# Optimization experiments

Hardware: AMD Instinct MI355X
Metric: run time of the kernel (lower is better)

Reference implementation:

```python
import jax, jax.numpy as jnp
import numpy as np

HEAD_DIM = 128  # dim // num_heads; RoPE rot_dim and softmax scale
ROPE_THETA = 10000.0


def rope_rotate(x, rot_dim):
    # lucidrains RotaryEmbedding.rotate_queries_or_keys: rotate first rot_dim
    # channels of last axis with interleaved-pair rotation; pass rest through.
    T = x.shape[-2]
    inv_freq = 1.0 / (ROPE_THETA ** (jnp.arange(0, rot_dim, 2, dtype=jnp.float32) / rot_dim))
    freqs = jnp.arange(T, dtype=jnp.float32)[:, None] * inv_freq[None, :]  # [T, rot_dim//2]
    freqs = jnp.repeat(freqs, 2, axis=-1)  # [T, rot_dim] interleaved (f0,f0,f1,f1,...)
    cos, sin = jnp.cos(freqs), jnp.sin(freqs)
    xr, x_pass = x[..., :rot_dim], x[..., rot_dim:]
    x1, x2 = xr[..., 0::2], xr[..., 1::2]
    rot = jnp.stack([-x2, x1], axis=-1).reshape(xr.shape)  # rotate_half
    xr = xr * cos + rot * sin
    return jnp.concatenate([xr, x_pass], axis=-1)


def setup_inputs() -> dict:
    key = jax.random.key(0)
    ks = jax.random.split(key, 9)
    B, T, D = 2, 2048, 2048
    w = lambda k, shape: jax.random.normal(k, shape, dtype=jnp.float32) * 0.02
    return {
        "latent_space": jax.random.normal(ks[0], (B, T, D), dtype=jnp.float32),
        "Wq": w(ks[1], (D, D)), "bq": w(ks[2], (D,)),
        "Wk": w(ks[3], (D, D)), "bk": w(ks[4], (D,)),
        "Wv": w(ks[5], (D, D)), "bv": w(ks[6], (D,)),
        "Wfc": w(ks[7], (D, D)), "bfc": w(ks[8], (D,)),
    }


def reference(latent_space, Wq, bq, Wk, bk, Wv, bv, Wfc, bfc):
    # Projections (nn.Linear: x @ W.T + b)
    Q = latent_space @ Wq.T + bq
    K = latent_space @ Wk.T + bk
    V = latent_space @ Wv.T + bv
    # Fused RoPE on first HEAD_DIM channels (module never splits heads)
    Q = rope_rotate(Q, HEAD_DIM)
    K = rope_rotate(K, HEAD_DIM)
    # Full-hidden-dim QK^T: [B,T,T]
    qk = jnp.einsum('btd,bsd->bts', Q, K)
    T = qk.shape[-1]
    causal = jnp.triu(jnp.ones((T, T), dtype=bool), 1)
    A = jnp.where(causal, -jnp.inf, qk)
    # PartialSoftmax with temp=1, h_t=None: state = A/sqrt(head_dim);
    # out = exp(state)/sum(exp(state)) * 2
    state = A / jnp.sqrt(jnp.float32(HEAD_DIM))
    x_exp = jnp.exp(state)
    A = x_exp / jnp.sum(x_exp, axis=-1, keepdims=True) * 2.0
    out = jnp.einsum('bts,bsd->btd', A, V) @ Wfc.T + bfc
    return out
```

## Files before the change

kernel.cpp:

```cpp
#include <hip/hip_runtime.h>
#include <hip/hip_bf16.h>
#include <math.h>

using bf16 = __hip_bfloat16;
typedef __attribute__((ext_vector_type(8))) __bf16 bf16x8;
typedef __attribute__((ext_vector_type(4))) float f32x4;

#define SBAR() asm volatile("s_barrier" ::: "memory")
#define WAITVM(n) asm volatile("s_waitcnt vmcnt(" #n ")" ::: "memory")

static __device__ __forceinline__ void gload16(const bf16* g, bf16* l) {
  __builtin_amdgcn_global_load_lds((const __attribute__((address_space(1))) void*)g,
                                   (__attribute__((address_space(3))) void*)l, 16, 0, 0);
}

struct POff { long a[4]; long b[4]; long c[4]; const float* bias[4]; };
struct CvtP { const float* s[5]; bf16* d[5]; int n4[5]; };

__global__ __launch_bounds__(256) void cvt_f32_bf16(CvtP p) {
  const int y = blockIdx.y;
  const int i = blockIdx.x * 256 + threadIdx.x;
  if (i >= p.n4[y]) return;
  const float4 v = reinterpret_cast<const float4*>(p.s[y])[i];
  union { bf16 h[4]; short4 s4; } u;
  u.h[0] = __float2bfloat16(v.x);
  u.h[1] = __float2bfloat16(v.y);
  u.h[2] = __float2bfloat16(v.z);
  u.h[3] = __float2bfloat16(v.w);
  *reinterpret_cast<short4*>(p.d[y] + 4 * (size_t)i) = u.s4;
}

template<bool BIAS, bool F32OUT, bool CAUSAL, bool KTRUNC>
__global__ __launch_bounds__(512, 2) void gemm_nt(
    const bf16* __restrict__ A, const bf16* __restrict__ B, char* __restrict__ Cv,
    POff P, int K, int lda, int ldb, int ldc)
{
  if (CAUSAL && (int)blockIdx.x > 2 * (int)blockIdx.y + 1) return;
  const int z = blockIdx.z;
  A = (const bf16*)((const char*)A + P.a[z]);
  B = (const bf16*)((const char*)B + P.b[z]);
  char* C = Cv + P.c[z];
  const int by = KTRUNC ? ((int)gridDim.y - 1 - (int)blockIdx.y) : (int)blockIdx.y;
  const int rowBase = by * 256;
  const int colBase = blockIdx.x * 128;
  const int tid  = threadIdx.x;
  const int lane = tid & 63;
  const int wid  = tid >> 6;
  const int wm = wid >> 1;
  const int wn = wid & 1;
  const int kEnd = KTRUNC ? (rowBase + 256) : K;
  const int NT = kEnd >> 5;

  __shared__ alignas(16) bf16 ls[4][12288];

  f32x4 acc[4][4] = {};

  const int rt  = tid >> 2;
  const int sw8 = ((tid & 3) ^ ((rt >> 1) & 3)) * 8;
  const bf16* gA0 = A + (size_t)(rowBase + rt) * lda + sw8;
  const bf16* gA1 = gA0 + (size_t)128 * lda;
  const bf16* gB0 = B + (size_t)(colBase + rt) * ldb + sw8;

  const int lr = lane >> 4, lc = lane & 15;
  const int kb = (lr ^ ((lc >> 1) & 3)) * 8;

#define STAGE(t) { bf16* d = &ls[(t) & 3][0]; const int ko = (t) * 32; \
    gload16(gA0 + ko, &d[tid * 8]); \
    gload16(gA1 + ko, &d[4096 + tid * 8]); \
    gload16(gB0 + ko, &d[8192 + tid * 8]); }

  STAGE(0); STAGE(1); STAGE(2);

  for (int t = 0; t < NT; ++t) {
    if (t < NT - 2)       WAITVM(6);
    else if (t == NT - 2) WAITVM(3);
    else                  WAITVM(0);
    SBAR();
    const bf16* LA = &ls[t & 3][0];
    const bf16* LB = &ls[t & 3][8192];
    bf16x8 af[4], bfr[4];
#pragma unroll
    for (int m = 0; m < 4; ++m)
      af[m] = *reinterpret_cast<const bf16x8*>(&LA[(wm * 64 + m * 16 + lc) * 32 + kb]);
#pragma unroll
    for (int n = 0; n < 4; ++n)
      bfr[n] = *reinterpret_cast<const bf16x8*>(&LB[(wn * 64 + n * 16 + lc) * 32 + kb]);
    if (t + 3 < NT) STAGE(t + 3);
    SBAR();
    __builtin_amdgcn_s_setprio(1);
#pragma unroll
    for (int m = 0; m < 4; ++m)
#pragma unroll
      for (int n = 0; n < 4; ++n)
        acc[m][n] = __builtin_amdgcn_mfma_f32_16x16x32_bf16(af[m], bfr[n], acc[m][n], 0, 0, 0);
    __builtin_amdgcn_s_setprio(0);
  }
#undef STAGE

  const float* bias = P.bias[z];
  const int crow0 = rowBase + wm * 64;
  const int ccol0 = colBase + wn * 64;
#pragma unroll
  for (int m = 0; m < 4; ++m) {
    const int row0 = crow0 + m * 16 + lr * 4;
#pragma unroll
    for (int n = 0; n < 4; ++n) {
      const int col = ccol0 + n * 16 + lc;
      const float bv = BIAS ? bias[col] : 0.f;
#pragma unroll
      for (int j = 0; j < 4; ++j) {
        const float v = acc[m][n][j] + bv;
        const long idx = (long)(row0 + j) * ldc + col;
        if (F32OUT) reinterpret_cast<float*>(C)[idx] = v;
        else        reinterpret_cast<bf16*>(C)[idx] = __float2bfloat16(v);
      }
    }
  }
}

__global__ __launch_bounds__(256) void rope_bf16(bf16* __restrict__ X) {
  const int idx = blockIdx.x * 256 + threadIdx.x;
  const int row = idx >> 6;
  const int i   = idx & 63;
  const int t   = row & 2047;
  const float ang = (float)t * exp2f((float)i * -0.20762050593046f);
  float sn, cs;
  sincosf(ang, &sn, &cs);
  bf16* p = X + ((long)row << 11) + 2 * i;
  const float x1 = __bfloat162float(p[0]);
  const float x2 = __bfloat162float(p[1]);
  p[0] = __float2bfloat16(x1 * cs - x2 * sn);
  p[1] = __float2bfloat16(x2 * cs + x1 * sn);
}

__global__ __launch_bounds__(256) void softmax_causal(
    const float* __restrict__ S0, const float* __restrict__ S1,
    const float* __restrict__ S2, const float* __restrict__ S3,
    bf16* __restrict__ A0, bf16* __restrict__ A1) {
  const int t = blockIdx.x;
  const int b = blockIdx.y;
  const float* ra = (b ? S2 : S0) + (long)t * 2048;
  const float* rb = (b ? S3 : S1) + (long)t * 2048;
  bf16* orow = (b ? A1 : A0) + (long)t * 4096;
  const int L = t + 1;
  __shared__ float e[2048];
  __shared__ float red[4];
  const float scale = 0.0883883476483184f;
  const int lane = threadIdx.x & 63, wd = threadIdx.x >> 6;

  float mx = -INFINITY;
  for (int s = threadIdx.x; s < L; s += 256) {
    const float v = (ra[s] + rb[s]) * scale;
    e[s] = v;
    mx = fmaxf(mx, v);
  }
#pragma unroll
  for (int off = 1; off < 64; off <<= 1) mx = fmaxf(mx, __shfl_xor(mx, off));
  if (lane == 0) red[wd] = mx;
  __syncthreads();
  mx = fmaxf(fmaxf(red[0], red[1]), fmaxf(red[2], red[3]));
  __syncthreads();

  float sum = 0.f;
  for (int s = threadIdx.x; s < L; s += 256) {
    const float v = expf(e[s] - mx);
    e[s] = v;
    sum += v;
  }
#pragma unroll
  for (int off = 1; off < 64; off <<= 1) sum += __shfl_xor(sum, off);
  if (lane == 0) red[wd] = sum;
  __syncthreads();
  sum = red[0] + red[1] + red[2] + red[3];
  const float f = 2.f / sum;
  for (int s = threadIdx.x; s < 2048; s += 256) {
    const float v = (s < L) ? e[s] * f : 0.f;
    orow[s] = __float2bfloat16(v);
  }
}

__global__ __launch_bounds__(256) void transpose_bf16(
    const bf16* __restrict__ V, bf16* __restrict__ VT) {
  __shared__ bf16 tile[32][33];
  const long b = blockIdx.z;
  const int s0 = blockIdx.y * 32, d0 = blockIdx.x * 32;
  const int tx = threadIdx.x;
  const int ty = threadIdx.y;
  for (int i = ty; i < 32; i += 8)
    tile[i][tx] = V[(b * 2048 + s0 + i) * 2048 + d0 + tx];
  __syncthreads();
  for (int i = ty; i < 32; i += 8)
    VT[(b * 2048 + d0 + i) * 2048 + s0 + tx] = tile[tx][i];
}

extern "C" void kernel_launch(void* const* d_in, const int* in_sizes, int n_in,
                              void* d_out, int out_size, void* d_ws, size_t ws_size,
                              hipStream_t stream) {
  (void)in_sizes; (void)n_in; (void)out_size; (void)ws_size;
  const float* lat = (const float*)d_in[0];
  const float* Wq  = (const float*)d_in[1];
  const float* bq  = (const float*)d_in[2];
  const float* Wk  = (const float*)d_in[3];
  const float* bk  = (const float*)d_in[4];
  const float* Wv  = (const float*)d_in[5];
  const float* bv  = (const float*)d_in[6];
  const float* Wfc = (const float*)d_in[7];
  const float* bfc = (const float*)d_in[8];
  float* out = (float*)d_out;

  constexpr long T = 2048, D = 2048, MT = 4096;
  constexpr long TTB = T * T * 4;
  char* w = (char*)d_ws;
  bf16* latb = (bf16*)w;  w += MT * D * 2;
  bf16* wqb  = (bf16*)w;  w += D * D * 2;
  bf16* wkb  = (bf16*)w;  w += D * D * 2;
  bf16* wvb  = (bf16*)w;  w += D * D * 2;
  bf16* wfb  = (bf16*)w;  w += D * D * 2;
  bf16* Qb   = (bf16*)w;  w += MT * D * 2;
  bf16* Kb   = (bf16*)w;  w += MT * D * 2;
  bf16* Vb   = (bf16*)w;  w += MT * D * 2;
  bf16* VTb  = (bf16*)w;  w += MT * D * 2;
  float* S0  = (float*)w; w += TTB;
  float* S1  = (float*)w; w += TTB;
  float* S2  = (float*)d_out;
  float* S3  = (float*)((char*)d_out + TTB);
  bf16* A0   = (bf16*)S0;
  bf16* A1   = (bf16*)S3;
  bf16* Ob   = latb;

  CvtP cp;
  cp.s[0] = lat; cp.d[0] = latb; cp.n4[0] = (int)(MT * D / 4);
  cp.s[1] = Wq;  cp.d[1] = wqb;  cp.n4[1] = (int)(D * D / 4);
  cp.s[2] = Wk;  cp.d[2] = wkb;  cp.n4[2] = (int)(D * D / 4);
  cp.s[3] = Wv;  cp.d[3] = wvb;  cp.n4[3] = (int)(D * D / 4);
  cp.s[4] = Wfc; cp.d[4] = wfb;  cp.n4[4] = (int)(D * D / 4);
  cvt_f32_bf16<<<dim3(8192, 5), 256, 0, stream>>>(cp);

  POff pq = {};
  for (int z = 0; z < 3; ++z) {
    pq.a[z] = 0;
    pq.b[z] = (long)z * D * D * 2;
    pq.c[z] = (long)z * MT * D * 2;
  }
  pq.bias[0] = bq; pq.bias[1] = bk; pq.bias[2] = bv;
  gemm_nt<true,false,false,false><<<dim3(16, 16, 3), 512, 0, stream>>>(
      latb, wqb, (char*)Qb, pq, 2048, 2048, 2048, 2048);

  rope_bf16<<<2048, 256, 0, stream>>>(Qb);

  POff ps = {};
  for (int z = 0; z < 4; ++z) {
    ps.a[z] = (long)(z >> 1) * T * D * 2 + (long)(z & 1) * 1024 * 2;
    ps.b[z] = ps.a[z];
  }
  ps.c[0] = 0;
  ps.c[1] = TTB;
  ps.c[2] = (char*)S2 - (char*)S0;
  ps.c[3] = (char*)S3 - (char*)S0;
  gemm_nt<false,true,true,false><<<dim3(16, 8, 4), 512, 0, stream>>>(
      Qb, Kb, (char*)S0, ps, 1024, 2048, 2048, 2048);

  softmax_causal<<<dim3(2048, 2), 256, 0, stream>>>(S0, S1, S2, S3, A0, A1);

  transpose_bf16<<<dim3(64, 64, 2), dim3(32, 8), 0, stream>>>(Vb, VTb);

  POff pv = {};
  pv.a[0] = 0; pv.a[1] = (char*)A1 - (char*)A0;
  pv.b[0] = 0; pv.b[1] = (long)D * T * 2;
  pv.c[0] = 0; pv.c[1] = (long)T * D * 2;
  gemm_nt<false,false,false,true><<<dim3(16, 8, 2), 512, 0, stream>>>(
      (const bf16*)A0, VTb, (char*)Ob, pv, 2048, 4096, 2048, 2048);

  POff pf = {};
  pf.bias[0] = bfc;
  gemm_nt<true,true,false,false><<<dim3(16, 16, 1), 512, 0, stream>>>(
      Ob, wfb, (char*)out, pf, 2048, 2048, 2048, 2048);
}
```

Baseline: 289.9 us.

## Use 256x256 GEMM tiles with split-K, batch V^T projection with QK^T

Replaces the templated 256x128 GEMM with a single flag-driven 256x256-tile kernel that takes per-z pointer tables. V is now computed directly as V^T (Wv x latent^T with a row bias), which removes the separate transpose kernel, and this GEMM is launched in the same grid as the causal QK^T blocks. The PV and FC GEMMs are split along K into fp32 partial sums, which are combined by new reduce kernels. The larger tiles improve data reuse and the split-K raises parallelism, but they cost extra fp32 partial-sum traffic, lower occupancy (launch bounds of 1 block per SM) and two extra launches.

```diff
diff --git a/kernel.cpp b/kernel.cpp
--- a/kernel.cpp
+++ b/kernel.cpp
@@ -14,7 +14,11 @@
                                    (__attribute__((address_space(3))) void*)l, 16, 0, 0);
 }
 
-struct POff { long a[4]; long b[4]; long c[4]; const float* bias[4]; };
+struct GP {
+  const bf16* A[6]; const bf16* B[6]; char* C[6];
+  const float* bias[6];
+  int K[6], flags[6], ktOff[6];
+};
 struct CvtP { const float* s[5]; bf16* d[5]; int n4[5]; };
 
 __global__ __launch_bounds__(256) void cvt_f32_bf16(CvtP p) {
@@ -30,36 +34,37 @@
   *reinterpret_cast<short4*>(p.d[y] + 4 * (size_t)i) = u.s4;
 }
 
-template<bool BIAS, bool F32OUT, bool CAUSAL, bool KTRUNC>
-__global__ __launch_bounds__(512, 2) void gemm_nt(
-    const bf16* __restrict__ A, const bf16* __restrict__ B, char* __restrict__ Cv,
-    POff P, int K, int lda, int ldb, int ldc)
-{
-  if (CAUSAL && (int)blockIdx.x > 2 * (int)blockIdx.y + 1) return;
+__global__ __launch_bounds__(512, 1) void gemm8(GP P, int lda, int ldb, int ldc) {
   const int z = blockIdx.z;
-  A = (const bf16*)((const char*)A + P.a[z]);
-  B = (const bf16*)((const char*)B + P.b[z]);
-  char* C = Cv + P.c[z];
-  const int by = KTRUNC ? ((int)gridDim.y - 1 - (int)blockIdx.y) : (int)blockIdx.y;
+  const int fl = P.flags[z];
+  if ((fl & 1) && blockIdx.x > blockIdx.y) return;
+  const int by = (fl & 8) ? ((int)gridDim.y - 1 - (int)blockIdx.y) : (int)blockIdx.y;
   const int rowBase = by * 256;
-  const int colBase = blockIdx.x * 128;
+  const int colBase = (int)blockIdx.x * 256;
+  int kEnd = P.K[z];
+  if (fl & 8) {
+    const int lim = rowBase + 256 - P.ktOff[z];
+    kEnd = kEnd < lim ? kEnd : lim;
+    if (kEnd <= 0) return;
+  }
+  const int NT = kEnd >> 5;
+
   const int tid  = threadIdx.x;
   const int lane = tid & 63;
   const int wid  = tid >> 6;
-  const int wm = wid >> 1;
-  const int wn = wid & 1;
-  const int kEnd = KTRUNC ? (rowBase + 256) : K;
-  const int NT = kEnd >> 5;
-
-  __shared__ alignas(16) bf16 ls[4][12288];
-
-  f32x4 acc[4][4] = {};
+  const int wm = wid >> 2;
+  const int wn = wid & 3;
+
+  __shared__ alignas(16) bf16 ls[4][16384];
+
+  f32x4 acc[8][4] = {};
 
   const int rt  = tid >> 2;
   const int sw8 = ((tid & 3) ^ ((rt >> 1) & 3)) * 8;
-  const bf16* gA0 = A + (size_t)(rowBase + rt) * lda + sw8;
+  const bf16* gA0 = P.A[z] + (size_t)(rowBase + rt) * lda + sw8;
   const bf16* gA1 = gA0 + (size_t)128 * lda;
-  const bf16* gB0 = B + (size_t)(colBase + rt) * ldb + sw8;
+  const bf16* gB0 = P.B[z] + (size_t)(colBase + rt) * ldb + sw8;
+  const bf16* gB1 = gB0 + (size_t)128 * ldb;
 
   const int lr = lane >> 4, lc = lane & 15;
   const int kb = (lr ^ ((lc >> 1) & 3)) * 8;
@@ -67,21 +72,22 @@
 #define STAGE(t) { bf16* d = &ls[(t) & 3][0]; const int ko = (t) * 32; \
     gload16(gA0 + ko, &d[tid * 8]); \
     gload16(gA1 + ko, &d[4096 + tid * 8]); \
-    gload16(gB0 + ko, &d[8192 + tid * 8]); }
+    gload16(gB0 + ko, &d[8192 + tid * 8]); \
+    gload16(gB1 + ko, &d[12288 + tid * 8]); }
 
   STAGE(0); STAGE(1); STAGE(2);
 
   for (int t = 0; t < NT; ++t) {
-    if (t < NT - 2)       WAITVM(6);
-    else if (t == NT - 2) WAITVM(3);
+    if (t < NT - 2)       WAITVM(8);
+    else if (t == NT - 2) WAITVM(4);
     else                  WAITVM(0);
     SBAR();
     const bf16* LA = &ls[t & 3][0];
     const bf16* LB = &ls[t & 3][8192];
-    bf16x8 af[4], bfr[4];
-#pragma unroll
-    for (int m = 0; m < 4; ++m)
-      af[m] = *reinterpret_cast<const bf16x8*>(&LA[(wm * 64 + m * 16 + lc) * 32 + kb]);
+    bf16x8 af[8], bfr[4];
+#pragma unroll
+    for (int m = 0; m < 8; ++m)
+      af[m] = *reinterpret_cast<const bf16x8*>(&LA[(wm * 128 + m * 16 + lc) * 32 + kb]);
 #pragma unroll
     for (int n = 0; n < 4; ++n)
       bfr[n] = *reinterpret_cast<const bf16x8*>(&LB[(wn * 64 + n * 16 + lc) * 32 + kb]);
@@ -89,7 +95,7 @@
     SBAR();
     __builtin_amdgcn_s_setprio(1);
 #pragma unroll
-    for (int m = 0; m < 4; ++m)
+    for (int m = 0; m < 8; ++m)
 #pragma unroll
       for (int n = 0; n < 4; ++n)
         acc[m][n] = __builtin_amdgcn_mfma_f32_16x16x32_bf16(af[m], bfr[n], acc[m][n], 0, 0, 0);
@@ -98,20 +104,20 @@
 #undef STAGE
 
   const float* bias = P.bias[z];
-  const int crow0 = rowBase + wm * 64;
-  const int ccol0 = colBase + wn * 64;
-#pragma unroll
-  for (int m = 0; m < 4; ++m) {
-    const int row0 = crow0 + m * 16 + lr * 4;
+  char* C = P.C[z];
+#pragma unroll
+  for (int m = 0; m < 8; ++m) {
+    const int row0 = rowBase + wm * 128 + m * 16 + lr * 4;
 #pragma unroll
     for (int n = 0; n < 4; ++n) {
-      const int col = ccol0 + n * 16 + lc;
-      const float bv = BIAS ? bias[col] : 0.f;
+      const int col = colBase + wn * 64 + n * 16 + lc;
+      const float bcol = (bias && !(fl & 2)) ? bias[col] : 0.f;
 #pragma unroll
       for (int j = 0; j < 4; ++j) {
-        const float v = acc[m][n][j] + bv;
+        float v = acc[m][n][j] + bcol;
+        if (fl & 2) v += bias[row0 + j];
         const long idx = (long)(row0 + j) * ldc + col;
-        if (F32OUT) reinterpret_cast<float*>(C)[idx] = v;
+        if (fl & 4) reinterpret_cast<float*>(C)[idx] = v;
         else        reinterpret_cast<bf16*>(C)[idx] = __float2bfloat16(v);
       }
     }
@@ -179,18 +185,44 @@
   }
 }
 
-__global__ __launch_bounds__(256) void transpose_bf16(
-    const bf16* __restrict__ V, bf16* __restrict__ VT) {
-  __shared__ bf16 tile[32][33];
-  const long b = blockIdx.z;
-  const int s0 = blockIdx.y * 32, d0 = blockIdx.x * 32;
-  const int tx = threadIdx.x;
-  const int ty = threadIdx.y;
-  for (int i = ty; i < 32; i += 8)
-    tile[i][tx] = V[(b * 2048 + s0 + i) * 2048 + d0 + tx];
-  __syncthreads();
-  for (int i = ty; i < 32; i += 8)
-    VT[(b * 2048 + d0 + i) * 2048 + s0 + tx] = tile[tx][i];
+__global__ __launch_bounds__(256) void pv_reduce(
+    const float* __restrict__ p0a, const float* __restrict__ p0b,
+    const float* __restrict__ p1, bf16* __restrict__ O) {
+  const long i4 = (long)blockIdx.x * 256 + threadIdx.x;
+  const long g = i4 * 4;
+  const int b = (int)(g >> 22);
+  const long rem = g & ((1L << 22) - 1);
+  const int r = (int)(rem >> 11);
+  const float* p0 = b ? p0b : p0a;
+  float4 v = *reinterpret_cast<const float4*>(p0 + rem);
+  if (r >= 1024) {
+    const float4 w = *reinterpret_cast<const float4*>(
+        p1 + (long)b * (1024 * 2048) + (rem - (1L << 21)));
+    v.x += w.x; v.y += w.y; v.z += w.z; v.w += w.w;
+  }
+  union { bf16 h[4]; short4 s; } u;
+  u.h[0] = __float2bfloat16(v.x);
+  u.h[1] = __float2bfloat16(v.y);
+  u.h[2] = __float2bfloat16(v.z);
+  u.h[3] = __float2bfloat16(v.w);
+  *reinterpret_cast<short4*>(O + g) = u.s;
+}
+
+__global__ __launch_bounds__(256) void fc_reduce(
+    const float* __restrict__ pa, const float* __restrict__ pb,
+    const float* __restrict__ bias, float* __restrict__ out) {
+  const long i4 = (long)blockIdx.x * 256 + threadIdx.x;
+  const long g = i4 * 4;
+  const int col = (int)(g & 2047);
+  const float4 a = reinterpret_cast<const float4*>(pa)[i4];
+  const float4 b4 = reinterpret_cast<const float4*>(pb)[i4];
+  const float4 bv = *reinterpret_cast<const float4*>(bias + col);
+  float4 o;
+  o.x = a.x + b4.x + bv.x;
+  o.y = a.y + b4.y + bv.y;
+  o.z = a.z + b4.z + bv.z;
+  o.w = a.w + b4.w + bv.w;
+  reinterpret_cast<float4*>(out)[i4] = o;
 }
 
 extern "C" void kernel_launch(void* const* d_in, const int* in_sizes, int n_in,
@@ -218,15 +250,19 @@
   bf16* wfb  = (bf16*)w;  w += D * D * 2;
   bf16* Qb   = (bf16*)w;  w += MT * D * 2;
   bf16* Kb   = (bf16*)w;  w += MT * D * 2;
-  bf16* Vb   = (bf16*)w;  w += MT * D * 2;
   bf16* VTb  = (bf16*)w;  w += MT * D * 2;
   float* S0  = (float*)w; w += TTB;
   float* S1  = (float*)w; w += TTB;
+  float* P1w = (float*)w; w += TTB;
   float* S2  = (float*)d_out;
   float* S3  = (float*)((char*)d_out + TTB);
   bf16* A0   = (bf16*)S0;
   bf16* A1   = (bf16*)S3;
+  float* P0a = S1;
+  float* P0b = S2;
   bf16* Ob   = latb;
+  float* Pf0 = (float*)Qb;
+  float* Pf1 = S0;
 
   CvtP cp;
   cp.s[0] = lat; cp.d[0] = latb; cp.n4[0] = (int)(MT * D / 4);
@@ -236,43 +272,60 @@
   cp.s[4] = Wfc; cp.d[4] = wfb;  cp.n4[4] = (int)(D * D / 4);
   cvt_f32_bf16<<<dim3(8192, 5), 256, 0, stream>>>(cp);
 
-  POff pq = {};
-  for (int z = 0; z < 3; ++z) {
-    pq.a[z] = 0;
-    pq.b[z] = (long)z * D * D * 2;
-    pq.c[z] = (long)z * MT * D * 2;
-  }
-  pq.bias[0] = bq; pq.bias[1] = bk; pq.bias[2] = bv;
-  gemm_nt<true,false,false,false><<<dim3(16, 16, 3), 512, 0, stream>>>(
-      latb, wqb, (char*)Qb, pq, 2048, 2048, 2048, 2048);
+  {
+    GP P = {};
+    P.A[0] = latb; P.B[0] = wqb; P.C[0] = (char*)Qb; P.bias[0] = bq; P.K[0] = 2048;
+    P.A[1] = latb; P.B[1] = wkb; P.C[1] = (char*)Kb; P.bias[1] = bk; P.K[1] = 2048;
+    gemm8<<<dim3(8, 16, 2), 512, 0, stream>>>(P, 2048, 2048, 2048);
+  }
 
   rope_bf16<<<2048, 256, 0, stream>>>(Qb);
 
-  POff ps = {};
-  for (int z = 0; z < 4; ++z) {
-    ps.a[z] = (long)(z >> 1) * T * D * 2 + (long)(z & 1) * 1024 * 2;
-    ps.b[z] = ps.a[z];
-  }
-  ps.c[0] = 0;
-  ps.c[1] = TTB;
-  ps.c[2] = (char*)S2 - (char*)S0;
-  ps.c[3] = (char*)S3 - (char*)S0;
-  gemm_nt<false,true,true,false><<<dim3(16, 8, 4), 512, 0, stream>>>(
-      Qb, Kb, (char*)S0, ps, 1024, 2048, 2048, 2048);
+  {
+    GP P = {};
+    for (int b = 0; b < 2; ++b) {
+      P.A[b] = wvb; P.B[b] = latb + (long)b * T * D;
+      P.C[b] = (char*)(VTb + (long)b * T * D);
+      P.bias[b] = bv; P.K[b] = 2048; P.flags[b] = 2;
+    }
+    char* sc[4] = {(char*)S0, (char*)S1, (char*)S2, (char*)S3};
+    for (int zz = 0; zz < 4; ++zz) {
+      const int b = zz >> 1, kh = zz & 1;
+      P.A[2 + zz] = Qb + (long)b * T * D + kh * 1024;
+      P.B[2 + zz] = Kb + (long)b * T * D + kh * 1024;
+      P.C[2 + zz] = sc[zz];
+      P.K[2 + zz] = 1024; P.flags[2 + zz] = 1 | 4;
+    }
+    gemm8<<<dim3(8, 8, 6), 512, 0, stream>>>(P, 2048, 2048, 2048);
+  }
 
   softmax_causal<<<dim3(2048, 2), 256, 0, stream>>>(S0, S1, S2, S3, A0, A1);
 
-  transpose_bf16<<<dim3(64, 64, 2), dim3(32, 8), 0, stream>>>(Vb, VTb);
-
-  POff pv = {};
-  pv.a[0] = 0; pv.a[1] = (char*)A1 - (char*)A0;
-  pv.b[0] = 0; pv.b[1] = (long)D * T * 2;
-  pv.c[0] = 0; pv.c[1] = (long)T * D * 2;
-  gemm_nt<false,false,false,true><<<dim3(16, 8, 2), 512, 0, stream>>>(
-      (const bf16*)A0, VTb, (char*)Ob, pv, 2048, 4096, 2048, 2048);
-
-  POff pf = {};
-  pf.bias[0] = bfc;
-  gemm_nt<true,true,false,false><<<dim3(16, 16, 1), 512, 0, stream>>>(
-      Ob, wfb, (char*)out, pf, 2048, 2048, 2048, 2048);
-}
+  {
+    GP P = {};
+    for (int z = 0; z < 4; ++z) {
+      const int b = z >> 1, kh = z & 1;
+      P.A[z] = (b ? A1 : A0) + kh * 1024;
+      P.B[z] = VTb + (long)b * T * D + kh * 1024;
+      P.C[z] = kh ? ((char*)P1w + (long)b * 1024 * 2048 * 4 - (long)1024 * 2048 * 4)
+                  : (char*)(b ? P0b : P0a);
+      P.K[z] = 1024; P.flags[z] = 8 | 4; P.ktOff[z] = kh * 1024;
+    }
+    gemm8<<<dim3(8, 8, 4), 512, 0, stream>>>(P, 4096, 2048, 2048);
+  }
+
+  pv_reduce<<<8192, 256, 0, stream>>>(P0a, P0b, P1w, Ob);
+
+  {
+    GP P = {};
+    for (int kh = 0; kh < 2; ++kh) {
+      P.A[kh] = Ob + kh * 1024;
+      P.B[kh] = wfb + kh * 1024;
+      P.C[kh] = (char*)(kh ? Pf1 : Pf0);
+      P.K[kh] = 1024; P.flags[kh] = 4;
+    }
+    gemm8<<<dim3(8, 16, 2), 512, 0, stream>>>(P, 2048, 2048, 2048);
+  }
+
+  fc_reduce<<<8192, 256, 0, stream>>>(Pf0, Pf1, bfc, out);
+}
```

Result: slower. 303.2 us (+4.6%).
